# Kernel optimization log

Measured on AMD Instinct MI355X. Metric: run time of the kernel, lower is better.

Reference implementation:

```python
import jax, jax.numpy as jnp
import numpy as np

N, E, T = 50000, 800000, 12
H, HEADS, L, O = 128, 4, 3, 12
C = H // HEADS
NEG_SLOPE = 0.2
LN_EPS = 1e-5


def setup_inputs() -> dict:
    key = jax.random.key(0)
    ks = iter(jax.random.split(key, 32))
    rn = lambda shape, s=0.1: jax.random.normal(next(ks), shape, jnp.float32) * s
    return {
        "x": rn((N, T), 1.0),
        "edge_index": jax.random.randint(next(ks), (2, E), 0, N, dtype=jnp.int32),
        "edge_attr": jax.random.uniform(next(ks), (E, 1), jnp.float32),
        "gru_Wih0": rn((3 * H, 1)), "gru_Whh0": rn((3 * H, H)),
        "gru_bih0": rn((3 * H,)), "gru_bhh0": rn((3 * H,)),
        "gru_Wih1": rn((3 * H, H)), "gru_Whh1": rn((3 * H, H)),
        "gru_bih1": rn((3 * H,)), "gru_bhh1": rn((3 * H,)),
        "gat_Wl": rn((L, H, H)), "gat_bl": rn((L, H)),
        "gat_Wr": rn((L, H, H)), "gat_br": rn((L, H)),
        "gat_We": rn((L, 1, H)),
        "gat_att": rn((L, HEADS, C)),
        "gat_bias": rn((L, H)),
        "ln_gamma": jnp.ones((L, H), jnp.float32),
        "ln_beta": jnp.zeros((L, H), jnp.float32),
        "fc_W1": rn((H, H)), "fc_b1": rn((H,)),
        "fc_W2": rn((H, O)), "fc_b2": rn((O,)),
    }


def _gru_layer(xs, Wih, Whh, bih, bhh):
    # xs: [T, N, D] time-major. Standard torch GRU cell math.
    gx = jnp.einsum('tnd,gd->tng', xs, Wih) + bih  # [T, N, 3H]
    h0 = jnp.zeros((xs.shape[1], H), xs.dtype)

    def step(h, g):
        gh = h @ Whh.T + bhh
        r = jax.nn.sigmoid(g[:, :H] + gh[:, :H])
        z = jax.nn.sigmoid(g[:, H:2 * H] + gh[:, H:2 * H])
        n = jnp.tanh(g[:, 2 * H:] + r * gh[:, 2 * H:])
        h_new = (1.0 - z) * n + z * h
        return h_new, h_new

    hT, hs = jax.lax.scan(step, h0, gx)
    return hT, hs


def _gatv2(x, src, dst, edge_attr, Wl, bl, Wr, br, We, att, bias):
    # GATv2Conv with edge features, no self loops, concat heads.
    xl = (x @ Wl + bl).reshape(N, HEADS, C)   # source transform (x_j)
    xr = (x @ Wr + br).reshape(N, HEADS, C)   # target transform (x_i)
    ee = (edge_attr @ We).reshape(-1, HEADS, C)
    m = xl[src] + xr[dst] + ee                # [E, HEADS, C]
    s = jnp.sum(jax.nn.leaky_relu(m, NEG_SLOPE) * att, axis=-1)  # [E, HEADS]
    smax = jax.lax.stop_gradient(jax.ops.segment_max(s, dst, num_segments=N))
    es = jnp.exp(s - smax[dst])
    denom = jax.ops.segment_sum(es, dst, num_segments=N)
    alpha = es / jnp.maximum(denom[dst], 1e-16)
    out = jax.ops.segment_sum(alpha[:, :, None] * xl[src], dst, num_segments=N)
    return out.reshape(N, H) + bias


def _layernorm(x, g, b):
    mu = jnp.mean(x, -1, keepdims=True)
    var = jnp.var(x, -1, keepdims=True)
    return (x - mu) * jax.lax.rsqrt(var + LN_EPS) * g + b


def _forward(x, edge_index, edge_attr,
             gru_Wih0, gru_Whh0, gru_bih0, gru_bhh0,
             gru_Wih1, gru_Whh1, gru_bih1, gru_bhh1,
             gat_Wl, gat_bl, gat_Wr, gat_br, gat_We, gat_att, gat_bias,
             ln_gamma, ln_beta, fc_W1, fc_b1, fc_W2, fc_b2):
    # Temporal: 2-layer GRU over the window, take final hidden of top layer.
    xs = x.T[:, :, None]                                  # [T, N, 1]
    _, hs0 = _gru_layer(xs, gru_Wih0, gru_Whh0, gru_bih0, gru_bhh0)
    h, _ = _gru_layer(hs0, gru_Wih1, gru_Whh1, gru_bih1, gru_bhh1)  # [N, H]

    src, dst = edge_index[0], edge_index[1]
    for l in range(L):
        res = h
        z = _gatv2(h, src, dst, edge_attr,
                   gat_Wl[l], gat_bl[l], gat_Wr[l], gat_br[l],
                   gat_We[l], gat_att[l], gat_bias[l])
        z = _layernorm(z, ln_gamma[l], ln_beta[l])
        h = jax.nn.elu(z) + res                           # dropout off (eval)

    h1 = jax.nn.relu(h @ fc_W1 + fc_b1)
    return h1 @ fc_W2 + fc_b2                             # [N, O]


def reference(x, edge_index, edge_attr,
              gru_Wih0, gru_Whh0, gru_bih0, gru_bhh0,
              gru_Wih1, gru_Whh1, gru_bih1, gru_bhh1,
              gat_Wl, gat_bl, gat_Wr, gat_br, gat_We, gat_att, gat_bias,
              ln_gamma, ln_beta, fc_W1, fc_b1, fc_W2, fc_b2):
    return _forward(x, edge_index, edge_attr,
                    gru_Wih0, gru_Whh0, gru_bih0, gru_bhh0,
                    gru_Wih1, gru_Whh1, gru_bih1, gru_bhh1,
                    gat_Wl, gat_bl, gat_Wr, gat_br, gat_We, gat_att, gat_bias,
                    ln_gamma, ln_beta, fc_W1, fc_b1, fc_W2, fc_b2)
```

## Files before the change

kernel.cpp:

```cpp
#include <hip/hip_runtime.h>

#define NN 50000
#define EE 800000
#define TT 12
#define HH 128
#define LLAYERS 3
#define OO 12

#define GRU_TILES 782
#define GRU_GRID  768

typedef __attribute__((ext_vector_type(8))) short short8;
typedef __attribute__((ext_vector_type(4))) float float4v;
typedef unsigned short ushort_t;

#define MFMA_BF16 __builtin_amdgcn_mfma_f32_16x16x32_bf16

#define L2E  1.4426950408889634f
#define L2E2 2.8853900817779268f

#if __has_builtin(__builtin_amdgcn_exp2f)
#define EXP2(x) __builtin_amdgcn_exp2f(x)
#else
#define EXP2(x) __expf((x) * 0.6931471805599453f)
#endif

__device__ __forceinline__ ushort_t f2b(float f) {
    union { float f; unsigned u; } v; v.f = f;
    unsigned u = v.u;
    return (ushort_t)((u + 0x7FFFu + ((u >> 16) & 1u)) >> 16);
}
__device__ __forceinline__ float b2f(ushort_t b) {
    union { unsigned u; float f; } v; v.u = ((unsigned)b) << 16; return v.f;
}
__device__ __forceinline__ short8 ld8(const ushort_t* p) { return *(const short8*)p; }

__device__ __forceinline__ float rcpf_(float x) { return __builtin_amdgcn_rcpf(x); }
__device__ __forceinline__ float sig2(float y) { return rcpf_(1.f + EXP2(-y)); }
__device__ __forceinline__ float tanh2(float y) {
    return fmaf(2.f, rcpf_(1.f + EXP2(-y)), -1.f);
}

__device__ __forceinline__ short8 lds_frag(const ushort_t* tile, int row, int kb) {
    int off = (row << 8) + kb;
    off ^= (row & 7) << 4;
    return *(const short8*)((const char*)tile + off);
}
__device__ __forceinline__ void lds_wr16(ushort_t* tile, int row, int cb, ushort_t v) {
    int off = (row << 8) + cb;
    off ^= (row & 7) << 4;
    *(ushort_t*)((char*)tile + off) = v;
}

#define MSTRIDE 132

__global__ __launch_bounds__(512, 2)
void gru_all(const float* __restrict__ x,
             const ushort_t* __restrict__ Whh0b, const float* __restrict__ Wih0,
             const float* __restrict__ bih0, const float* __restrict__ bhh0,
             const ushort_t* __restrict__ Wih1b, const ushort_t* __restrict__ Whh1b,
             const float* __restrict__ bih1, const float* __restrict__ bhh1,
             float* __restrict__ h1f, ushort_t* __restrict__ h1b,
             const int* __restrict__ src, const int* __restrict__ dst,
             const float* __restrict__ ea, int* __restrict__ cursor,
             int2* __restrict__ edgeS) {
    __shared__ ushort_t h0sA[9216], h0sB[9216], h1sA[9216], h1sB[9216];
    __shared__ float h0m[64 * MSTRIDE], h1m[64 * MSTRIDE];
    __shared__ float xsh[768];

    if (blockIdx.x >= GRU_GRID) {
        int e = (blockIdx.x - GRU_GRID) * 512 + threadIdx.x;
        if (e < EE) {
            int pos = atomicAdd(&cursor[dst[e]], 1);
            edgeS[pos] = make_int2(src[e], __float_as_int(ea[e]));
        }
        return;
    }

    const int tid = threadIdx.x;
    const int wv = tid >> 6, lane = tid & 63;
    const int cl = lane & 15, kg = lane >> 4;
    const int jj = wv * 16 + cl;

    short8 w0[3][4], wxx[3][4], whh[3][4];
#pragma unroll
    for (int g = 0; g < 3; ++g)
#pragma unroll
        for (int ks = 0; ks < 4; ++ks) {
            const size_t ro = (size_t)(g * 128 + jj) * HH + ks * 32 + kg * 8;
            w0[g][ks]  = ld8(Whh0b + ro);
            wxx[g][ks] = ld8(Wih1b + ro);
            whh[g][ks] = ld8(Whh1b + ro);
        }
    const float wiR = Wih0[jj] * L2E, wiZ = Wih0[jj + 128] * L2E, wiN = Wih0[jj + 256] * L2E2;
    const float b0R = (bih0[jj] + bhh0[jj]) * L2E;
    const float b0Z = (bih0[jj + 128] + bhh0[jj + 128]) * L2E;
    const float b0N = bih0[jj + 256] * L2E2;
    const float c0N = bhh0[jj + 256] * L2E2;
    const float b1R = (bih1[jj] + bhh1[jj]) * L2E;
    const float b1Z = (bih1[jj + 128] + bhh1[jj + 128]) * L2E;
    const float b1N = bih1[jj + 256] * L2E2;
    const float c1N = bhh1[jj + 256] * L2E2;

    const int rdl = kg * 288 + cl * 16;
    const int ksw = jj >> 5;
    const int kcw = (jj >> 3) & 3;
    const int wbase = (ksw * 16 + kcw) * 288 + kg * 64 + (jj & 7) * 2;

#pragma unroll 1
    for (int tile = blockIdx.x; tile < GRU_TILES; tile += GRU_GRID) {
        const int r0 = tile * 64;

        for (int q = tid; q < 768; q += 512) {
            int tt = q >> 6, row = q & 63;
            int node = r0 + row;
            xsh[q] = (node < NN) ? x[(size_t)node * TT + tt] : 0.f;
        }
        for (int q = tid; q < 4608; q += 512) {
            ((unsigned*)h0sA)[q] = 0u; ((unsigned*)h1sA)[q] = 0u;
        }
        for (int q = tid; q < 64 * MSTRIDE; q += 512) { h0m[q] = 0.f; h1m[q] = 0.f; }
        __syncthreads();

        ushort_t* h0c = h0sA; ushort_t* h0n = h0sB;
        ushort_t* h1c = h1sA; ushort_t* h1n = h1sB;

#pragma unroll 1
        for (int t = 0; t < TT; ++t) {
            const float* xrow = xsh + t * 64;
#pragma unroll 2
            for (int rt = 0; rt < 4; ++rt) {
                short8 a[4];
#pragma unroll
                for (int ks = 0; ks < 4; ++ks)
                    a[ks] = *(const short8*)((const char*)h0c + ks * 4608 + rt * 1152 + rdl);
                float4v aR = {0,0,0,0}, aZ = {0,0,0,0}, aN = {0,0,0,0};
#pragma unroll
                for (int ks = 0; ks < 4; ++ks) {
                    aR = MFMA_BF16(a[ks], w0[0][ks], aR, 0, 0, 0);
                    aZ = MFMA_BF16(a[ks], w0[1][ks], aZ, 0, 0, 0);
                    aN = MFMA_BF16(a[ks], w0[2][ks], aN, 0, 0, 0);
                }
#pragma unroll
                for (int i = 0; i < 4; ++i) {
                    const int rl = rt * 16 + kg * 4 + i;
                    float xv = xrow[rl];
                    float hold = h0m[rl * MSTRIDE + jj];
                    float r = sig2(fmaf(xv, wiR, b0R) + aR[i]);
                    float z = sig2(fmaf(xv, wiZ, b0Z) + aZ[i]);
                    float nn2 = tanh2(fmaf(xv, wiN, b0N) + r * (aN[i] + c0N));
                    float hn = fmaf(z, hold - nn2, nn2);
                    h0m[rl * MSTRIDE + jj] = hn;
                    *(ushort_t*)((char*)h0n + wbase + rt * 1152 + i * 16) = f2b(hn);
                }
            }
            __syncthreads();
#pragma unroll 2
            for (int rt = 0; rt < 4; ++rt) {
                short8 an[4], a1[4];
#pragma unroll
                for (int ks = 0; ks < 4; ++ks) {
                    an[ks] = *(const short8*)((const char*)h0n + ks * 4608 + rt * 1152 + rdl);
                    a1[ks] = *(const short8*)((const char*)h1c + ks * 4608 + rt * 1152 + rdl);
                }
                float4v gR = {0,0,0,0}, gZ = {0,0,0,0}, xN = {0,0,0,0}, hN = {0,0,0,0};
#pragma unroll
                for (int ks = 0; ks < 4; ++ks) {
                    gR = MFMA_BF16(an[ks], wxx[0][ks], gR, 0, 0, 0);
                    gZ = MFMA_BF16(an[ks], wxx[1][ks], gZ, 0, 0, 0);
                    xN = MFMA_BF16(an[ks], wxx[2][ks], xN, 0, 0, 0);
                    gR = MFMA_BF16(a1[ks], whh[0][ks], gR, 0, 0, 0);
                    gZ = MFMA_BF16(a1[ks], whh[1][ks], gZ, 0, 0, 0);
                    hN = MFMA_BF16(a1[ks], whh[2][ks], hN, 0, 0, 0);
                }
#pragma unroll
                for (int i = 0; i < 4; ++i) {
                    const int rl = rt * 16 + kg * 4 + i;
                    float hold = h1m[rl * MSTRIDE + jj];
                    float r = sig2(gR[i] + b1R);
                    float z = sig2(gZ[i] + b1Z);
                    float nn2 = tanh2(xN[i] + b1N + r * (hN[i] + c1N));
                    float hn = fmaf(z, hold - nn2, nn2);
                    h1m[rl * MSTRIDE + jj] = hn;
                    *(ushort_t*)((char*)h1n + wbase + rt * 1152 + i * 16) = f2b(hn);
                }
            }
            ushort_t* tmp0 = h0c; h0c = h0n; h0n = tmp0;
            ushort_t* tmp1 = h1c; h1c = h1n; h1n = tmp1;
        }

#pragma unroll
        for (int rt = 0; rt < 4; ++rt)
#pragma unroll
            for (int i = 0; i < 4; ++i) {
                const int rl = rt * 16 + kg * 4 + i;
                int node = r0 + rl;
                if (node < NN) {
                    float v = h1m[rl * MSTRIDE + jj];
                    const size_t off = (size_t)node * HH + jj;
                    h1f[off] = v;
                    h1b[off] = f2b(v);
                }
            }
        __syncthreads();
    }
}

__global__ __launch_bounds__(256)
void gemm_dual(const ushort_t* __restrict__ A,
               const ushort_t* __restrict__ B1, const ushort_t* __restrict__ B2,
               const float* __restrict__ bias1, const float* __restrict__ bias2,
               ushort_t* __restrict__ C1, ushort_t* __restrict__ C2) {
    const int wave = threadIdx.x >> 6, lane = threadIdx.x & 63;
    const int r0 = (blockIdx.x * 4 + wave) * 32;
    const int col = lane & 15, kg = lane >> 4;
    const int arow0 = min(r0 + col, NN - 1);
    const int arow1 = min(r0 + 16 + col, NN - 1);
    short8 a0[4], a1[4];
#pragma unroll
    for (int ks = 0; ks < 4; ++ks) {
        a0[ks] = ld8(A + (size_t)arow0 * HH + ks * 32 + kg * 8);
        a1[ks] = ld8(A + (size_t)arow1 * HH + ks * 32 + kg * 8);
    }
#pragma unroll
    for (int j0 = 0; j0 < 8; ++j0) {
        float4v c10 = {0,0,0,0}, c11 = {0,0,0,0}, c20 = {0,0,0,0}, c21 = {0,0,0,0};
        const ushort_t* p1 = B1 + (size_t)(j0 * 16 + col) * HH + kg * 8;
        const ushort_t* p2 = B2 + (size_t)(j0 * 16 + col) * HH + kg * 8;
#pragma unroll
        for (int ks = 0; ks < 4; ++ks) {
            short8 b1v = ld8(p1 + ks * 32);
            short8 b2v = ld8(p2 + ks * 32);
            c10 = MFMA_BF16(a0[ks], b1v, c10, 0, 0, 0);
            c11 = MFMA_BF16(a1[ks], b1v, c11, 0, 0, 0);
            c20 = MFMA_BF16(a0[ks], b2v, c20, 0, 0, 0);
            c21 = MFMA_BF16(a1[ks], b2v, c21, 0, 0, 0);
        }
        const int jj = j0 * 16 + col;
        const float b1 = bias1[jj], b2 = bias2[jj];
#pragma unroll
        for (int i = 0; i < 4; ++i) {
            int node0 = r0 + kg * 4 + i;
            int node1 = node0 + 16;
            if (node0 < NN) {
                C1[(size_t)node0 * HH + jj] = f2b(c10[i] + b1);
                C2[(size_t)node0 * HH + jj] = f2b(c20[i] + b2);
            }
            if (node1 < NN) {
                C1[(size_t)node1 * HH + jj] = f2b(c11[i] + b1);
                C2[(size_t)node1 * HH + jj] = f2b(c21[i] + b2);
            }
        }
    }
}

__global__ void csr_alloc(const int* __restrict__ deg, int2* __restrict__ rbdeg,
                          int* __restrict__ cursor, int* __restrict__ gcnt) {
    int n = blockIdx.x * 256 + threadIdx.x;
    int ln = threadIdx.x & 63;
    int d = (n < NN) ? deg[n] : 0;
    int s = d;
#pragma unroll
    for (int off = 1; off < 64; off <<= 1) {
        int t = __shfl_up(s, off);
        if (ln >= off) s += t;
    }
    int base = 0;
    if (ln == 63) base = atomicAdd(gcnt, s);
    base = __shfl(base, 63);
    int excl = base + s - d;
    if (n < NN) { rbdeg[n] = make_int2(excl, d); cursor[n] = excl; }
}

__global__ __launch_bounds__(256)
void gat_fused(const int2* __restrict__ rbdeg,
               const int2* __restrict__ edgeS,
               const ushort_t* __restrict__ xlb, const ushort_t* __restrict__ xrb,
               const float* __restrict__ We, const float* __restrict__ att,
               const float* __restrict__ gbias, const float* __restrict__ gamma,
               const float* __restrict__ beta,
               float* __restrict__ h1f, ushort_t* __restrict__ h1b) {
    const int node = (blockIdx.x * 256 + threadIdx.x) >> 6;
    const int lane = threadIdx.x & 63;
    if (node >= NN) return;
    const int g = lane >> 4, gl = lane & 15;
    const int cb = gl * 8;

    short8 xrv = ld8(xrb + (size_t)node * HH + cb);
    float xr[8], Wv[8], Av[8];
#pragma unroll
    for (int c = 0; c < 8; ++c) xr[c] = b2f((ushort_t)xrv[c]);
    *(float4*)&Wv[0] = *(const float4*)(We + cb);
    *(float4*)&Wv[4] = *(const float4*)(We + cb + 4);
    *(float4*)&Av[0] = *(const float4*)(att + cb);
    *(float4*)&Av[4] = *(const float4*)(att + cb + 4);

    const int2 bd = rbdeg[node];
    const int beg = bd.x;
    const int end = beg + bd.y;
    float acc[8] = {};
    float den = 0.f;

    if (beg < end) {
        bool valid = (beg + g) < end;
        int es = min(beg + g, end - 1);
        int2 ed = edgeS[es];
        short8 xlv = ld8(xlb + (size_t)ed.x * HH + cb);
        for (int base = beg; base < end; base += 4) {
            int nbase = base + 4;
            int2 ed2 = ed; short8 xlv2 = {};
            bool nvalid = false;
            if (nbase < end) {
                nvalid = (nbase + g) < end;
                int nes = min(nbase + g, end - 1);
                ed2 = edgeS[nes];
                xlv2 = ld8(xlb + (size_t)ed2.x * HH + cb);
            }
            float ev = __int_as_float(ed.y);
            float xl[8];
            float p = 0.f;
#pragma unroll
            for (int c = 0; c < 8; ++c) {
                xl[c] = b2f((ushort_t)xlv[c]);
                float m = xl[c] + xr[c] + ev * Wv[c];
                m = (m > 0.f) ? m : 0.2f * m;
                p = fmaf(m, Av[c], p);
            }
            p += __shfl_xor(p, 1);
            p += __shfl_xor(p, 2);
            float w = valid ? __expf(p) : 0.f;
            den += w;
#pragma unroll
            for (int c = 0; c < 8; ++c) acc[c] = fmaf(w, xl[c], acc[c]);
            valid = nvalid; ed = ed2; xlv = xlv2;
        }
    }
#pragma unroll
    for (int c = 0; c < 8; ++c) {
        acc[c] += __shfl_xor(acc[c], 16);
        acc[c] += __shfl_xor(acc[c], 32);
    }
    den += __shfl_xor(den, 16);
    den += __shfl_xor(den, 32);

    float invd = 1.f / fmaxf(den, 1e-16f);
    float gb[8];
    *(float4*)&gb[0] = *(const float4*)(gbias + cb);
    *(float4*)&gb[4] = *(const float4*)(gbias + cb + 4);
    float o[8], s1 = 0.f, s2 = 0.f;
#pragma unroll
    for (int c = 0; c < 8; ++c) {
        o[c] = acc[c] * invd + gb[c];
        s1 += o[c];
        s2 = fmaf(o[c], o[c], s2);
    }
#pragma unroll
    for (int d = 1; d < 16; d <<= 1) {
        s1 += __shfl_xor(s1, d);
        s2 += __shfl_xor(s2, d);
    }
    float mean = s1 * (1.f / 128.f);
    float var = s2 * (1.f / 128.f) - mean * mean;
    float inv = rsqrtf(var + 1e-5f);

    if (g == 0) {
        float gm[8], bt[8], hv[8];
        *(float4*)&gm[0] = *(const float4*)(gamma + cb);
        *(float4*)&gm[4] = *(const float4*)(gamma + cb + 4);
        *(float4*)&bt[0] = *(const float4*)(beta + cb);
        *(float4*)&bt[4] = *(const float4*)(beta + cb + 4);
        *(float4*)&hv[0] = *(const float4*)(h1f + (size_t)node * HH + cb);
        *(float4*)&hv[4] = *(const float4*)(h1f + (size_t)node * HH + cb + 4);
        short8 pk;
#pragma unroll
        for (int c = 0; c < 8; ++c) {
            float y = (o[c] - mean) * inv * gm[c] + bt[c];
            y = (y > 0.f) ? y : expm1f(y);
            hv[c] += y;
            pk[c] = (short)f2b(hv[c]);
        }
        *(float4*)(h1f + (size_t)node * HH + cb)     = *(float4*)&hv[0];
        *(float4*)(h1f + (size_t)node * HH + cb + 4) = *(float4*)&hv[4];
        *(short8*)(h1b + (size_t)node * HH + cb) = pk;
    }
}

__global__ __launch_bounds__(256)
void fc_head(const ushort_t* __restrict__ A, const ushort_t* __restrict__ W1b,
             const float* __restrict__ b1, const ushort_t* __restrict__ W2b,
             const float* __restrict__ b2, float* __restrict__ out) {
    __shared__ ushort_t hs[4][4096];
    const int wave = threadIdx.x >> 6, lane = threadIdx.x & 63;
    const int r0 = (blockIdx.x * 4 + wave) * 32;
    const int col = lane & 15, kg = lane >> 4;
    const int arow0 = min(r0 + col, NN - 1);
    const int arow1 = min(r0 + 16 + col, NN - 1);
    short8 a0[4], a1[4];
#pragma unroll
    for (int ks = 0; ks < 4; ++ks) {
        a0[ks] = ld8(A + (size_t)arow0 * HH + ks * 32 + kg * 8);
        a1[ks] = ld8(A + (size_t)arow1 * HH + ks * 32 + kg * 8);
    }
#pragma unroll
    for (int j0 = 0; j0 < 8; ++j0) {
        float4v acc0 = {0,0,0,0}, acc1 = {0,0,0,0};
        const ushort_t* bp = W1b + (size_t)(j0 * 16 + col) * HH + kg * 8;
#pragma unroll
        for (int ks = 0; ks < 4; ++ks) {
            short8 bv = ld8(bp + ks * 32);
            acc0 = MFMA_BF16(a0[ks], bv, acc0, 0, 0, 0);
            acc1 = MFMA_BF16(a1[ks], bv, acc1, 0, 0, 0);
        }
        const int jj = j0 * 16 + col;
        const float bj = b1[jj];
#pragma unroll
        for (int i = 0; i < 4; ++i) {
            lds_wr16(hs[wave], kg * 4 + i, jj * 2, f2b(fmaxf(acc0[i] + bj, 0.f)));
            lds_wr16(hs[wave], 16 + kg * 4 + i, jj * 2, f2b(fmaxf(acc1[i] + bj, 0.f)));
        }
    }
    short8 w2f[4];
#pragma unroll
    for (int ks = 0; ks < 4; ++ks)
        w2f[ks] = ld8(W2b + (size_t)col * HH + ks * 32 + kg * 8);
#pragma unroll
    for (int rh = 0; rh < 2; ++rh) {
        short8 f[4];
#pragma unroll
        for (int ks = 0; ks < 4; ++ks)
            f[ks] = lds_frag(hs[wave], rh * 16 + col, ks * 64 + kg * 16);
        float4v acc2 = {0,0,0,0};
#pragma unroll
        for (int ks = 0; ks < 4; ++ks)
            acc2 = MFMA_BF16(f[ks], w2f[ks], acc2, 0, 0, 0);
        if (col < OO) {
            const float bj = b2[col];
#pragma unroll
            for (int i = 0; i < 4; ++i) {
                int node = r0 + rh * 16 + kg * 4 + i;
                if (node < NN) out[(size_t)node * OO + col] = acc2[i] + bj;
            }
        }
    }
}

__global__ void conv_cnt(const float* __restrict__ Whh0, const float* __restrict__ Wih1,
                         const float* __restrict__ Whh1, const float* __restrict__ gWl,
                         const float* __restrict__ gWr, const float* __restrict__ fcW1,
                         const float* __restrict__ fcW2,
                         ushort_t* __restrict__ Whh0b, ushort_t* __restrict__ Wih1b,
                         ushort_t* __restrict__ Whh1b, ushort_t* __restrict__ WlTb,
                         ushort_t* __restrict__ WrTb, ushort_t* __restrict__ W1Tb,
                         ushort_t* __restrict__ W2Tb,
                         const int* __restrict__ dst, int* __restrict__ deg) {
    if (blockIdx.x >= 1032) {
        int e = (blockIdx.x - 1032) * 256 + threadIdx.x;
        if (e < EE) atomicAdd(&deg[dst[e]], 1);
        return;
    }
    int idx = blockIdx.x * 256 + threadIdx.x;
    if (idx < 147456) {
        const float* s; ushort_t* d; int o = idx;
        if (o < 49152)        { s = Whh0; d = Whh0b; }
        else if (o < 98304)   { s = Wih1; d = Wih1b; o -= 49152; }
        else                  { s = Whh1; d = Whh1b; o -= 98304; }
        float scale = (o >= 256 * 128) ? L2E2 : L2E;
        d[o] = f2b(s[o] * scale);
    } else if (idx < 262144) {
        int local = idx - 147456;
        int mt = local >> 14, o = local & 16383;
        int r = o >> 7, c = o & 127;
        const float* s; ushort_t* d;
        if (mt < 3)      { s = gWl + (size_t)mt * 16384;       d = WlTb + (size_t)mt * 16384; }
        else if (mt < 6) { s = gWr + (size_t)(mt - 3) * 16384; d = WrTb + (size_t)(mt - 3) * 16384; }
        else             { s = fcW1;                            d = W1Tb; }
        d[c * 128 + r] = f2b(s[r * 128 + c]);
    } else if (idx < 264192) {
        int o = idx - 262144;
        int j = o >> 7, k = o & 127;
        W2Tb[o] = (j < OO) ? f2b(fcW2[k * OO + j]) : (ushort_t)0;
    }
}

extern "C" void kernel_launch(void* const* d_in, const int* in_sizes, int n_in,
                              void* d_out, int out_size, void* d_ws, size_t ws_size,
                              hipStream_t stream) {
    const float* x     = (const float*)d_in[0];
    const int*   ei    = (const int*)d_in[1];
    const int*   src   = ei;
    const int*   dst   = ei + EE;
    const float* ea    = (const float*)d_in[2];
    const float* Wih0  = (const float*)d_in[3];
    const float* Whh0  = (const float*)d_in[4];
    const float* bih0  = (const float*)d_in[5];
    const float* bhh0  = (const float*)d_in[6];
    const float* Wih1  = (const float*)d_in[7];
    const float* Whh1  = (const float*)d_in[8];
    const float* bih1  = (const float*)d_in[9];
    const float* bhh1  = (const float*)d_in[10];
    const float* gWl   = (const float*)d_in[11];
    const float* gbl   = (const float*)d_in[12];
    const float* gWr   = (const float*)d_in[13];
    const float* gbr   = (const float*)d_in[14];
    const float* gWe   = (const float*)d_in[15];
    const float* gatt  = (const float*)d_in[16];
    const float* gbias = (const float*)d_in[17];
    const float* lng   = (const float*)d_in[18];
    const float* lnb   = (const float*)d_in[19];
    const float* fcW1  = (const float*)d_in[20];
    const float* fcb1  = (const float*)d_in[21];
    const float* fcW2  = (const float*)d_in[22];
    const float* fcb2  = (const float*)d_in[23];
    float* out = (float*)d_out;
    float* ws  = (float*)d_ws;

    const size_t NH = (size_t)NN * HH;

    ushort_t* h1b   = (ushort_t*)ws;
    ushort_t* xlb   = h1b + NH;
    ushort_t* xrb   = xlb + NH;
    ushort_t* Whh0b = xrb + NH;
    ushort_t* Wih1b = Whh0b + 49152;
    ushort_t* Whh1b = Wih1b + 49152;
    ushort_t* WlTb  = Whh1b + 49152;
    ushort_t* WrTb  = WlTb + 49152;
    ushort_t* W1Tb  = WrTb + 49152;
    ushort_t* W2Tb  = W1Tb + 16384;

    float* p    = ws + (3 * NH + 5 * 49152 + 16384 + 2048) / 2;
    float* h1f  = p; p += NH;
    int* deg    = (int*)p;
    int2* rbdeg = (int2*)(deg + NN);
    int* cursor = (int*)(rbdeg + NN);
    int* gcnt   = cursor + NN;
    int2* edgeS = (int2*)(gcnt + 4);

    hipMemsetAsync(deg, 0, (size_t)NN * sizeof(int), stream);
    hipMemsetAsync(gcnt, 0, 4 * sizeof(int), stream);
    conv_cnt<<<1032 + (EE + 255) / 256, 256, 0, stream>>>(
        Whh0, Wih1, Whh1, gWl, gWr, fcW1, fcW2,
        Whh0b, Wih1b, Whh1b, WlTb, WrTb, W1Tb, W2Tb, dst, deg);

    csr_alloc<<<(NN + 255) / 256, 256, 0, stream>>>(deg, rbdeg, cursor, gcnt);

    const int fillBlocks = (EE + 511) / 512;
    gru_all<<<GRU_GRID + fillBlocks, 512, 0, stream>>>(
        x, Whh0b, Wih0, bih0, bhh0, Wih1b, Whh1b, bih1, bhh1, h1f, h1b,
        src, dst, ea, cursor, edgeS);

    const int dualBlocks = (NN + 127) / 128;
    const int fusedBlocks = (NN + 3) / 4;
    for (int l = 0; l < LLAYERS; ++l) {
        gemm_dual<<<dualBlocks, 256, 0, stream>>>(h1b, WlTb + (size_t)l * 16384,
                                                  WrTb + (size_t)l * 16384,
                                                  gbl + l * HH, gbr + l * HH, xlb, xrb);
        gat_fused<<<fusedBlocks, 256, 0, stream>>>(rbdeg, edgeS, xlb, xrb,
                                                   gWe + l * HH, gatt + l * HH,
                                                   gbias + l * HH, lng + l * HH, lnb + l * HH,
                                                   h1f, h1b);
    }

    fc_head<<<dualBlocks, 256, 0, stream>>>(h1b, W1Tb, fcb1, W2Tb, fcb2, out);
}
```

Baseline: 590.3 us.

## Bucket nodes by in-degree so GAT wavefronts process similar-degree nodes

Builds a degree histogram in csr_alloc and scans it in a new single-block kernel. Extra blocks in gru_all then counting-sort node ids by degree into a permutation array. gat_fused maps each wavefront slot through this permutation, so the four wavefronts of a block handle nodes of similar degree, which reduces load imbalance between them. The cost is an extra kernel launch, a histogram of atomics, and scattered access to node rows instead of consecutive nodes.

```diff
diff --git a/kernel.cpp b/kernel.cpp
--- a/kernel.cpp
+++ b/kernel.cpp
@@ -9,6 +9,8 @@
 
 #define GRU_TILES 782
 #define GRU_GRID  768
+#define FILLB     1563
+#define SORTB     98
 
 typedef __attribute__((ext_vector_type(8))) short short8;
 typedef __attribute__((ext_vector_type(4))) float float4v;
@@ -63,11 +65,22 @@
              float* __restrict__ h1f, ushort_t* __restrict__ h1b,
              const int* __restrict__ src, const int* __restrict__ dst,
              const float* __restrict__ ea, int* __restrict__ cursor,
-             int2* __restrict__ edgeS) {
+             int2* __restrict__ edgeS,
+             const int* __restrict__ deg, int* __restrict__ dcur,
+             int* __restrict__ perm) {
     __shared__ ushort_t h0sA[9216], h0sB[9216], h1sA[9216], h1sB[9216];
     __shared__ float h0m[64 * MSTRIDE], h1m[64 * MSTRIDE];
     __shared__ float xsh[768];
 
+    if (blockIdx.x >= GRU_GRID + FILLB) {
+        int n = (blockIdx.x - GRU_GRID - FILLB) * 512 + threadIdx.x;
+        if (n < NN) {
+            int b = min(deg[n], 511);
+            int pos = atomicAdd(&dcur[b], 1);
+            perm[pos] = n;
+        }
+        return;
+    }
     if (blockIdx.x >= GRU_GRID) {
         int e = (blockIdx.x - GRU_GRID) * 512 + threadIdx.x;
         if (e < EE) {
@@ -255,7 +268,8 @@
 }
 
 __global__ void csr_alloc(const int* __restrict__ deg, int2* __restrict__ rbdeg,
-                          int* __restrict__ cursor, int* __restrict__ gcnt) {
+                          int* __restrict__ cursor, int* __restrict__ gcnt,
+                          int* __restrict__ dhist) {
     int n = blockIdx.x * 256 + threadIdx.x;
     int ln = threadIdx.x & 63;
     int d = (n < NN) ? deg[n] : 0;
@@ -269,20 +283,46 @@
     if (ln == 63) base = atomicAdd(gcnt, s);
     base = __shfl(base, 63);
     int excl = base + s - d;
-    if (n < NN) { rbdeg[n] = make_int2(excl, d); cursor[n] = excl; }
+    if (n < NN) {
+        rbdeg[n] = make_int2(excl, d);
+        cursor[n] = excl;
+        atomicAdd(&dhist[min(d, 511)], 1);
+    }
+}
+
+__global__ __launch_bounds__(512)
+void dsort_scan(const int* __restrict__ dhist, int* __restrict__ dcur) {
+    __shared__ int wsum[8];
+    const int tid = threadIdx.x, ln = tid & 63, wv = tid >> 6;
+    int v = dhist[tid];
+    int s = v;
+#pragma unroll
+    for (int d = 1; d < 64; d <<= 1) { int t = __shfl_up(s, d); if (ln >= d) s += t; }
+    if (ln == 63) wsum[wv] = s;
+    __syncthreads();
+    if (tid < 8) {
+        int w = wsum[tid];
+#pragma unroll
+        for (int d = 1; d < 8; d <<= 1) { int u = __shfl_up(w, d); if (tid >= d) w += u; }
+        wsum[tid] = w;
+    }
+    __syncthreads();
+    int wof = wv ? wsum[wv - 1] : 0;
+    dcur[tid] = wof + s - v;
 }
 
 __global__ __launch_bounds__(256)
 void gat_fused(const int2* __restrict__ rbdeg,
-               const int2* __restrict__ edgeS,
+               const int2* __restrict__ edgeS, const int* __restrict__ perm,
                const ushort_t* __restrict__ xlb, const ushort_t* __restrict__ xrb,
                const float* __restrict__ We, const float* __restrict__ att,
                const float* __restrict__ gbias, const float* __restrict__ gamma,
                const float* __restrict__ beta,
                float* __restrict__ h1f, ushort_t* __restrict__ h1b) {
-    const int node = (blockIdx.x * 256 + threadIdx.x) >> 6;
+    const int slot = (blockIdx.x * 256 + threadIdx.x) >> 6;
     const int lane = threadIdx.x & 63;
-    if (node >= NN) return;
+    if (slot >= NN) return;
+    const int node = perm[slot];
     const int g = lane >> 4, gl = lane & 15;
     const int cb = gl * 8;
 
@@ -533,20 +573,24 @@
     int2* rbdeg = (int2*)(deg + NN);
     int* cursor = (int*)(rbdeg + NN);
     int* gcnt   = cursor + NN;
-    int2* edgeS = (int2*)(gcnt + 4);
+    int* dhist  = gcnt + 4;
+    int* dcur   = dhist + 512;
+    int* perm   = dcur + 512;
+    int* pad_   = perm + NN;
+    int2* edgeS = (int2*)(pad_ + ((NN & 1) ? 1 : 0) + 2);
 
     hipMemsetAsync(deg, 0, (size_t)NN * sizeof(int), stream);
-    hipMemsetAsync(gcnt, 0, 4 * sizeof(int), stream);
+    hipMemsetAsync(gcnt, 0, (4 + 512) * sizeof(int), stream);
     conv_cnt<<<1032 + (EE + 255) / 256, 256, 0, stream>>>(
         Whh0, Wih1, Whh1, gWl, gWr, fcW1, fcW2,
         Whh0b, Wih1b, Whh1b, WlTb, WrTb, W1Tb, W2Tb, dst, deg);
 
-    csr_alloc<<<(NN + 255) / 256, 256, 0, stream>>>(deg, rbdeg, cursor, gcnt);
-
-    const int fillBlocks = (EE + 511) / 512;
-    gru_all<<<GRU_GRID + fillBlocks, 512, 0, stream>>>(
+    csr_alloc<<<(NN + 255) / 256, 256, 0, stream>>>(deg, rbdeg, cursor, gcnt, dhist);
+    dsort_scan<<<1, 512, 0, stream>>>(dhist, dcur);
+
+    gru_all<<<GRU_GRID + FILLB + SORTB, 512, 0, stream>>>(
         x, Whh0b, Wih0, bih0, bhh0, Wih1b, Whh1b, bih1, bhh1, h1f, h1b,
-        src, dst, ea, cursor, edgeS);
+        src, dst, ea, cursor, edgeS, deg, dcur, perm);
 
     const int dualBlocks = (NN + 127) / 128;
     const int fusedBlocks = (NN + 3) / 4;
@@ -554,7 +598,7 @@
         gemm_dual<<<dualBlocks, 256, 0, stream>>>(h1b, WlTb + (size_t)l * 16384,
                                                   WrTb + (size_t)l * 16384,
                                                   gbl + l * HH, gbr + l * HH, xlb, xrb);
-        gat_fused<<<fusedBlocks, 256, 0, stream>>>(rbdeg, edgeS, xlb, xrb,
+        gat_fused<<<fusedBlocks, 256, 0, stream>>>(rbdeg, edgeS, perm, xlb, xrb,
                                                    gWe + l * HH, gatt + l * HH,
                                                    gbias + l * HH, lng + l * HH, lnb + l * HH,
                                                    h1f, h1b);
```

After: 865.0 us. 1.47x slower.
